# Optimization experiments

Hardware: AMD Instinct MI355X
Metric: run time of the kernel (lower is better)

Reference implementation:

```python
import jax, jax.numpy as jnp
import numpy as np

D_MODEL = 1024
N_EXPERTS = 8
CAPACITY = 2048


def setup_inputs() -> dict:
    key = jax.random.key(0)
    ks = jax.random.split(key, 8)
    D, E, H = D_MODEL, N_EXPERTS, 4 * D_MODEL
    s = lambda fan_in: 1.0 / np.sqrt(fan_in)
    return {
        "x": jax.random.normal(ks[0], (4, 2048, D), dtype=jnp.float32),
        "Wg": jax.random.uniform(ks[1], (D, E), minval=-s(D), maxval=s(D)),
        "bg": jax.random.uniform(ks[2], (E,), minval=-s(D), maxval=s(D)),
        "W1": jax.random.uniform(ks[3], (E, D, H), minval=-s(D), maxval=s(D)),
        "b1": jax.random.uniform(ks[4], (E, H), minval=-s(D), maxval=s(D)),
        "W2": jax.random.uniform(ks[5], (E, H, D), minval=-s(H), maxval=s(H)),
        "b2": jax.random.uniform(ks[6], (E, D), minval=-s(H), maxval=s(H)),
        "top_k": 1,
    }


def reference(x, Wg, bg, W1, b1, W2, b2, top_k):
    B, S, D = x.shape
    E, C = N_EXPERTS, CAPACITY
    x_flat = x.reshape(-1, D)                      # [N, D]
    N = x_flat.shape[0]

    # Router: top-k expert indices per token
    logits = x_flat @ Wg + bg                      # [N, E]
    _, routes = jax.lax.top_k(logits, top_k)       # [N, k]
    r = routes.reshape(-1)                         # [N*k] row-major, matches torch flatten order
    tok = jnp.repeat(jnp.arange(N), top_k)         # token id per routing slot

    # Position of each routed token within its expert's queue (arrival order)
    oh = (r[:, None] == jnp.arange(E)[None, :]).astype(jnp.int32)  # [N*k, E]
    pos = jnp.cumsum(oh, axis=0)[jnp.arange(r.shape[0]), r] - 1    # [N*k]
    kept = pos < C
    slot = jnp.where(kept, pos, C)                 # dropped tokens -> overflow slot C

    # Dispatch: gather tokens into per-expert padded buffers [E, C, D]
    disp = jnp.zeros((E, C + 1, D), dtype=x.dtype).at[r, slot].set(x_flat[tok])
    disp = disp[:, :C]

    # Per-expert MLP (grouped GEMMs)
    h = jax.nn.relu(jnp.einsum('ecd,edh->ech', disp, W1) + b1[:, None, :])
    y = jnp.einsum('ech,ehd->ecd', h, W2) + b2[:, None, :]  # [E, C, D]

    # Combine: scatter expert outputs back; dropped tokens stay zero
    gathered = y[r, jnp.minimum(pos, C - 1)]       # [N*k, D]
    out_flat = jnp.zeros((N, D), dtype=x.dtype).at[tok].set(
        jnp.where(kept[:, None], gathered, 0.0))
    return out_flat.reshape(B, S, D)
```

## Files before the change

kernel.cpp:

```cpp
#include <hip/hip_runtime.h>


#define N_TOK   8192
#define DMODEL  1024
#define HDIM    4096
#define NEXP    8
#define CAP     2048
#define MAXROWS 9216

typedef float  f32x4  __attribute__((ext_vector_type(4)));
typedef __bf16 bf16x8 __attribute__((ext_vector_type(8)));

typedef void __attribute__((address_space(1))) as1_void;
typedef void __attribute__((address_space(3))) as3_void;

__device__ __forceinline__ void async_copy16(void* lds, const void* g) {
    __builtin_amdgcn_global_load_lds((as1_void*)g, (as3_void*)lds, 16, 0, 0);
}

__device__ __forceinline__ unsigned short f2bf(float f) {
    unsigned u = __float_as_uint(f);
    unsigned r = (u + 0x7fffu + ((u >> 16) & 1u)) >> 16;
    return (unsigned short)r;
}

__global__ __launch_bounds__(256) void gate_kernel(
    const float* __restrict__ x, const float* __restrict__ Wg,
    const float* __restrict__ bg, int* __restrict__ route)
{
    const int wave = threadIdx.x >> 6, lane = threadIdx.x & 63;
    const int tok = blockIdx.x * 4 + wave;
    const float* xr = x + (size_t)tok * DMODEL;
    double acc[8];
#pragma unroll
    for (int e = 0; e < 8; ++e) acc[e] = 0.0;
    for (int i = 0; i < DMODEL / 64; ++i) {
        const int d = i * 64 + lane;
        const double xv = (double)xr[d];
        const float* wr = Wg + (size_t)d * 8;
#pragma unroll
        for (int e = 0; e < 8; ++e) acc[e] += xv * (double)wr[e];
    }
#pragma unroll
    for (int e = 0; e < 8; ++e) {
        double v = acc[e];
#pragma unroll
        for (int off = 32; off > 0; off >>= 1) v += __shfl_down(v, off, 64);
        acc[e] = v;
    }
    if (lane == 0) {
        double bv = acc[0] + (double)bg[0];
        int bi = 0;
#pragma unroll
        for (int e = 1; e < 8; ++e) {
            double v = acc[e] + (double)bg[e];
            if (v > bv) { bv = v; bi = e; }
        }
        route[tok] = bi;
    }
}

__global__ __launch_bounds__(256) void scan_kernel(
    const int* __restrict__ route, int* __restrict__ tokrow,
    int* __restrict__ meta)
{
    __shared__ int hist[256][8];
    __shared__ int cntS[8];
    __shared__ int rowbaseS[8];
    const int tid = threadIdx.x;
    for (int i = tid; i < MAXROWS; i += 256) tokrow[i] = -1;
    const int t0 = tid * 32;
    int r[32];
#pragma unroll
    for (int i = 0; i < 32; ++i) r[i] = route[t0 + i];
    int loc[8];
#pragma unroll
    for (int e = 0; e < 8; ++e) loc[e] = 0;
#pragma unroll
    for (int i = 0; i < 32; ++i) {
#pragma unroll
        for (int e = 0; e < 8; ++e) loc[e] += (r[i] == e) ? 1 : 0;
    }
#pragma unroll
    for (int e = 0; e < 8; ++e) hist[tid][e] = loc[e];
    __syncthreads();
    if (tid < 8) {
        int run = 0;
        for (int t = 0; t < 256; ++t) { int v = hist[t][tid]; hist[t][tid] = run; run += v; }
        meta[tid] = run;
        cntS[tid] = run;
    }
    __syncthreads();
    if (tid == 0) {
        int rb = 0;
#pragma unroll
        for (int e = 0; e < 8; ++e) {
            int c = cntS[e]; if (c > CAP) c = CAP;
            int p = (c + 127) & ~127;
            meta[8 + e] = p;
            meta[16 + e] = rb;
            rowbaseS[e] = rb;
            rb += p;
        }
        meta[24] = rb;
    }
    __syncthreads();
    int base[8];
#pragma unroll
    for (int e = 0; e < 8; ++e) base[e] = hist[tid][e];
#pragma unroll
    for (int i = 0; i < 32; ++i) {
        const int e = r[i];
        const int p = base[e]++;
        if (p < CAP) tokrow[rowbaseS[e] + p] = t0 + i;
    }
}

__global__ __launch_bounds__(256) void dispatch_kernel(
    const float* __restrict__ x, const int* __restrict__ tokrow,
    unsigned short* __restrict__ xg)
{
    const int row = blockIdx.x;
    const int tok = tokrow[row];
    const int d = threadIdx.x * 4;
    float4 v = make_float4(0.f, 0.f, 0.f, 0.f);
    if (tok >= 0) v = *(const float4*)(x + (size_t)tok * DMODEL + d);
    ushort4 o;
    o.x = f2bf(v.x); o.y = f2bf(v.y); o.z = f2bf(v.z); o.w = f2bf(v.w);
    *(ushort4*)(xg + (size_t)row * DMODEL + d) = o;
}

__global__ __launch_bounds__(256) void transpose_cast_kernel(
    const float* __restrict__ in, unsigned short* __restrict__ out,
    int R, int C)
{
    __shared__ float t[128][33];
    const size_t base = (size_t)blockIdx.z * R * C;
    const int c0 = blockIdx.x * 32, r0 = blockIdx.y * 128;
    const int x = threadIdx.x, y0 = threadIdx.y;
#pragma unroll
    for (int i = 0; i < 16; ++i) {
        const int r = y0 + i * 8;
        t[r][x] = in[base + (size_t)(r0 + r) * C + c0 + x];
    }
    __syncthreads();
#pragma unroll
    for (int j = 0; j < 4; ++j) {
        const int c = y0 + j * 8;
        ushort4 o;
        o.x = f2bf(t[4 * x + 0][c]);
        o.y = f2bf(t[4 * x + 1][c]);
        o.z = f2bf(t[4 * x + 2][c]);
        o.w = f2bf(t[4 * x + 3][c]);
        *(ushort4*)(&out[base + (size_t)(c0 + c) * R + r0 + 4 * x]) = o;
    }
}

__device__ __forceinline__ void mfma_mainloop(
    const unsigned short* __restrict__ A,
    const unsigned short* __restrict__ B,
    int K, int tid, char* smem, f32x4 acc[4][4])
{
    const int wave = tid >> 6, lane = tid & 63;
    const int mrow = lane >> 2;
    const int kofs = (lane & 3) * 8;
    const int quad = lane >> 4, l16 = lane & 15;
    const int wm = (wave & 1) * 64, wn = (wave >> 1) * 64;

    for (int k0 = 0; k0 < K; k0 += 32) {
        __syncthreads();
#pragma unroll
        for (int i = 0; i < 2; ++i) {
            const int m = wave * 32 + i * 16 + mrow;
            async_copy16(smem + wave * 2048 + i * 1024 + lane * 16,
                         A + (size_t)m * K + k0 + kofs);
        }
#pragma unroll
        for (int i = 0; i < 2; ++i) {
            const int n = wave * 32 + i * 16 + mrow;
            async_copy16(smem + 8192 + wave * 2048 + i * 1024 + lane * 16,
                         B + (size_t)n * K + k0 + kofs);
        }
        __syncthreads();
        bf16x8 a[4], b[4];
#pragma unroll
        for (int mi = 0; mi < 4; ++mi)
            a[mi] = *(const bf16x8*)(smem + ((wm + mi * 16 + l16) * 32 + quad * 8) * 2);
#pragma unroll
        for (int ni = 0; ni < 4; ++ni)
            b[ni] = *(const bf16x8*)(smem + 8192 + ((wn + ni * 16 + l16) * 32 + quad * 8) * 2);
#pragma unroll
        for (int mi = 0; mi < 4; ++mi)
#pragma unroll
            for (int ni = 0; ni < 4; ++ni)
                acc[mi][ni] = __builtin_amdgcn_mfma_f32_16x16x32_bf16(
                    a[mi], b[ni], acc[mi][ni], 0, 0, 0);
    }
}

__global__ __launch_bounds__(256) void gemm1_kernel(
    const unsigned short* __restrict__ xg,
    const unsigned short* __restrict__ wb,
    const float* __restrict__ b1,
    unsigned short* __restrict__ hbuf,
    const int* __restrict__ meta)
{
    const int lin = blockIdx.x + 32 * (blockIdx.y + 16 * blockIdx.z);
    const int work = (lin & 7) * 512 + (lin >> 3);
    const int e = work >> 9;
    const int rem = work & 511;
    const int mtile = rem & 15, ntile = rem >> 4;
    if (mtile * 128 >= meta[8 + e]) return;
    const int row0 = meta[16 + e] + mtile * 128;
    const int tid = threadIdx.x;

    __shared__ __align__(16) char lds[32768];

    f32x4 acc[4][4];
#pragma unroll
    for (int mi = 0; mi < 4; ++mi)
#pragma unroll
        for (int ni = 0; ni < 4; ++ni)
#pragma unroll
            for (int r = 0; r < 4; ++r) acc[mi][ni][r] = 0.0f;

    mfma_mainloop(xg + (size_t)row0 * DMODEL,
                  wb + ((size_t)e * HDIM + (size_t)ntile * 128) * DMODEL,
                  DMODEL, tid, lds, acc);

    __syncthreads();
    unsigned short* hl = (unsigned short*)lds;
    const int wave = tid >> 6, lane = tid & 63;
    const int quad = lane >> 4, l16 = lane & 15;
    const int wm = (wave & 1) * 64, wn = (wave >> 1) * 64;
    const float* bias = b1 + (size_t)e * HDIM + (size_t)ntile * 128;
#pragma unroll
    for (int mi = 0; mi < 4; ++mi)
#pragma unroll
        for (int ni = 0; ni < 4; ++ni) {
            const int cc = wn + ni * 16 + l16;
            const float bv = bias[cc];
#pragma unroll
            for (int r = 0; r < 4; ++r) {
                const int rr = wm + mi * 16 + quad * 4 + r;
                hl[rr * 128 + cc] = f2bf(fmaxf(acc[mi][ni][r] + bv, 0.0f));
            }
        }
    __syncthreads();
#pragma unroll
    for (int i = 0; i < 8; ++i) {
        const int c = tid + i * 256;
        const int m = c >> 4;
        const int nb = (c & 15) * 8;
        *(int4*)(hbuf + (size_t)(row0 + m) * HDIM + (size_t)ntile * 128 + nb) =
            *(const int4*)(hl + m * 128 + nb);
    }
}

__global__ __launch_bounds__(256) void gemm2_kernel(
    const unsigned short* __restrict__ hbuf,
    const unsigned short* __restrict__ wb,
    const float* __restrict__ b2,
    const int* __restrict__ tokrow,
    float* __restrict__ out,
    const int* __restrict__ meta)
{
    const int lin = blockIdx.x + 8 * (blockIdx.y + 16 * blockIdx.z);
    const int work = (lin & 7) * 128 + (lin >> 3);
    const int e = work >> 7;
    const int rem = work & 127;
    const int mtile = rem & 15, ntile = rem >> 4;
    if (mtile * 128 >= meta[8 + e]) return;
    const int row0 = meta[16 + e] + mtile * 128;
    const int tid = threadIdx.x;

    __shared__ __align__(16) char lds[16384];

    f32x4 acc[4][4];
#pragma unroll
    for (int mi = 0; mi < 4; ++mi)
#pragma unroll
        for (int ni = 0; ni < 4; ++ni)
#pragma unroll
            for (int r = 0; r < 4; ++r) acc[mi][ni][r] = 0.0f;

    mfma_mainloop(hbuf + (size_t)row0 * HDIM,
                  wb + ((size_t)e * DMODEL + (size_t)ntile * 128) * HDIM,
                  HDIM, tid, lds, acc);

    const int wave = tid >> 6, lane = tid & 63;
    const int quad = lane >> 4, l16 = lane & 15;
    const int wm = (wave & 1) * 64, wn = (wave >> 1) * 64;
#pragma unroll
    for (int mi = 0; mi < 4; ++mi) {
#pragma unroll
        for (int r = 0; r < 4; ++r) {
            const int rowl = wm + mi * 16 + quad * 4 + r;
            const int tok = tokrow[row0 + rowl];
            if (tok >= 0) {
#pragma unroll
                for (int ni = 0; ni < 4; ++ni) {
                    const int col = ntile * 128 + wn + ni * 16 + l16;
                    out[(size_t)tok * DMODEL + col] =
                        acc[mi][ni][r] + b2[(size_t)e * DMODEL + col];
                }
            }
        }
    }
}

extern "C" void kernel_launch(void* const* d_in, const int* in_sizes, int n_in,
                              void* d_out, int out_size, void* d_ws, size_t ws_size,
                              hipStream_t stream) {
    (void)in_sizes; (void)n_in; (void)out_size; (void)ws_size;
    const float* x  = (const float*)d_in[0];
    const float* Wg = (const float*)d_in[1];
    const float* bg = (const float*)d_in[2];
    const float* W1 = (const float*)d_in[3];
    const float* b1 = (const float*)d_in[4];
    const float* W2 = (const float*)d_in[5];
    const float* b2 = (const float*)d_in[6];
    float* out = (float*)d_out;
    char* ws = (char*)d_ws;

    int* route  = (int*)ws;
    int* tokrow = (int*)(ws + 32768);
    int* meta   = (int*)(ws + 69632);
    unsigned short* xg   = (unsigned short*)(ws + (size_t)131072);
    unsigned short* hbuf = (unsigned short*)(ws + (size_t)20 * 1024 * 1024);
    unsigned short* wb   = (unsigned short*)(ws + (size_t)96 * 1024 * 1024);

    hipMemsetAsync(d_out, 0, (size_t)N_TOK * DMODEL * sizeof(float), stream);

    gate_kernel<<<N_TOK / 4, 256, 0, stream>>>(x, Wg, bg, route);
    scan_kernel<<<1, 256, 0, stream>>>(route, tokrow, meta);
    dispatch_kernel<<<MAXROWS, 256, 0, stream>>>(x, tokrow, xg);

    transpose_cast_kernel<<<dim3(HDIM / 32, DMODEL / 128, NEXP), dim3(32, 8), 0, stream>>>(
        W1, wb, DMODEL, HDIM);
    gemm1_kernel<<<dim3(HDIM / 128, 16, NEXP), 256, 0, stream>>>(
        xg, wb, b1, hbuf, meta);

    transpose_cast_kernel<<<dim3(DMODEL / 32, HDIM / 128, NEXP), dim3(32, 8), 0, stream>>>(
        W2, wb, HDIM, DMODEL);
    gemm2_kernel<<<dim3(DMODEL / 128, 16, NEXP), 256, 0, stream>>>(
        hbuf, wb, b2, tokrow, out, meta);
}
```

Before: 581.1 us.

## Double-buffer GEMM K-loop with BK=64, XOR-swizzled LDS, and vectorized transpose

The shared GEMM mainloop moves from a single 32-wide K tile with two barriers per step to a double-buffered 64-wide K tile. The next tile is loaded asynchronously while the current one is computed, and the LDS layout uses an XOR swizzle to avoid bank conflicts. The weight transpose-cast kernel now uses 64x64 tiles with float4 global loads. LDS per block grows to 64KB, which may reduce occupancy.

Result: slower. 605.1 us (+4.1%).

```diff
diff --git a/kernel.cpp b/kernel.cpp
--- a/kernel.cpp
+++ b/kernel.cpp
@@ -134,25 +134,72 @@
     const float* __restrict__ in, unsigned short* __restrict__ out,
     int R, int C)
 {
-    __shared__ float t[128][33];
+    __shared__ float t[64][65];
     const size_t base = (size_t)blockIdx.z * R * C;
-    const int c0 = blockIdx.x * 32, r0 = blockIdx.y * 128;
-    const int x = threadIdx.x, y0 = threadIdx.y;
-#pragma unroll
-    for (int i = 0; i < 16; ++i) {
-        const int r = y0 + i * 8;
-        t[r][x] = in[base + (size_t)(r0 + r) * C + c0 + x];
-    }
-    __syncthreads();
-#pragma unroll
-    for (int j = 0; j < 4; ++j) {
-        const int c = y0 + j * 8;
+    const int c0 = blockIdx.x * 64, r0 = blockIdx.y * 64;
+    const int tid = threadIdx.x;
+    const int rl = tid >> 4;
+    const int cl = (tid & 15) * 4;
+#pragma unroll
+    for (int i = 0; i < 4; ++i) {
+        const int r = rl + i * 16;
+        const float4 v = *(const float4*)(in + base + (size_t)(r0 + r) * C + c0 + cl);
+        t[r][cl] = v.x; t[r][cl + 1] = v.y; t[r][cl + 2] = v.z; t[r][cl + 3] = v.w;
+    }
+    __syncthreads();
+#pragma unroll
+    for (int i = 0; i < 4; ++i) {
+        const int c = rl + i * 16;
         ushort4 o;
-        o.x = f2bf(t[4 * x + 0][c]);
-        o.y = f2bf(t[4 * x + 1][c]);
-        o.z = f2bf(t[4 * x + 2][c]);
-        o.w = f2bf(t[4 * x + 3][c]);
-        *(ushort4*)(&out[base + (size_t)(c0 + c) * R + r0 + 4 * x]) = o;
+        o.x = f2bf(t[cl + 0][c]);
+        o.y = f2bf(t[cl + 1][c]);
+        o.z = f2bf(t[cl + 2][c]);
+        o.w = f2bf(t[cl + 3][c]);
+        *(ushort4*)(out + base + (size_t)(c0 + c) * R + r0 + cl) = o;
+    }
+}
+
+__device__ __forceinline__ void stage_tile(
+    const unsigned short* __restrict__ A,
+    const unsigned short* __restrict__ B,
+    int K, int tid, char* bufA, char* bufB, int k0)
+{
+#pragma unroll
+    for (int i = 0; i < 4; ++i) {
+        const int c = tid + i * 256;
+        const int row = c >> 3;
+        const int g8 = ((c & 7) ^ (row & 7)) * 8;
+        async_copy16(bufA + (size_t)c * 16, A + (size_t)row * K + k0 + g8);
+    }
+#pragma unroll
+    for (int i = 0; i < 4; ++i) {
+        const int c = tid + i * 256;
+        const int row = c >> 3;
+        const int g8 = ((c & 7) ^ (row & 7)) * 8;
+        async_copy16(bufB + (size_t)c * 16, B + (size_t)row * K + k0 + g8);
+    }
+}
+
+__device__ __forceinline__ void compute_tile(
+    const char* bufA, const char* bufB,
+    int wm, int wn, int l16, int quad, f32x4 acc[4][4])
+{
+#pragma unroll
+    for (int ks = 0; ks < 2; ++ks) {
+        const int sc = ((ks * 4 + quad) ^ (l16 & 7)) * 16;
+        bf16x8 a[4], b[4];
+#pragma unroll
+        for (int mi = 0; mi < 4; ++mi)
+            a[mi] = *(const bf16x8*)(bufA + (wm + mi * 16 + l16) * 128 + sc);
+#pragma unroll
+        for (int ni = 0; ni < 4; ++ni)
+            b[ni] = *(const bf16x8*)(bufB + (wn + ni * 16 + l16) * 128 + sc);
+#pragma unroll
+        for (int mi = 0; mi < 4; ++mi)
+#pragma unroll
+            for (int ni = 0; ni < 4; ++ni)
+                acc[mi][ni] = __builtin_amdgcn_mfma_f32_16x16x32_bf16(
+                    a[mi], b[ni], acc[mi][ni], 0, 0, 0);
     }
 }
 
@@ -162,39 +209,23 @@
     int K, int tid, char* smem, f32x4 acc[4][4])
 {
     const int wave = tid >> 6, lane = tid & 63;
-    const int mrow = lane >> 2;
-    const int kofs = (lane & 3) * 8;
     const int quad = lane >> 4, l16 = lane & 15;
     const int wm = (wave & 1) * 64, wn = (wave >> 1) * 64;
-
-    for (int k0 = 0; k0 < K; k0 += 32) {
+    char* A0 = smem;
+    char* B0 = smem + 16384;
+    char* A1 = smem + 32768;
+    char* B1 = smem + 49152;
+
+    stage_tile(A, B, K, tid, A0, B0, 0);
+    __syncthreads();
+    const int nIter = K >> 6;
+    for (int it = 0; it < nIter; ++it) {
+        const bool odd = (it & 1) != 0;
+        if (it + 1 < nIter)
+            stage_tile(A, B, K, tid, odd ? A0 : A1, odd ? B0 : B1,
+                       (it + 1) << 6);
+        compute_tile(odd ? A1 : A0, odd ? B1 : B0, wm, wn, l16, quad, acc);
         __syncthreads();
-#pragma unroll
-        for (int i = 0; i < 2; ++i) {
-            const int m = wave * 32 + i * 16 + mrow;
-            async_copy16(smem + wave * 2048 + i * 1024 + lane * 16,
-                         A + (size_t)m * K + k0 + kofs);
-        }
-#pragma unroll
-        for (int i = 0; i < 2; ++i) {
-            const int n = wave * 32 + i * 16 + mrow;
-            async_copy16(smem + 8192 + wave * 2048 + i * 1024 + lane * 16,
-                         B + (size_t)n * K + k0 + kofs);
-        }
-        __syncthreads();
-        bf16x8 a[4], b[4];
-#pragma unroll
-        for (int mi = 0; mi < 4; ++mi)
-            a[mi] = *(const bf16x8*)(smem + ((wm + mi * 16 + l16) * 32 + quad * 8) * 2);
-#pragma unroll
-        for (int ni = 0; ni < 4; ++ni)
-            b[ni] = *(const bf16x8*)(smem + 8192 + ((wn + ni * 16 + l16) * 32 + quad * 8) * 2);
-#pragma unroll
-        for (int mi = 0; mi < 4; ++mi)
-#pragma unroll
-            for (int ni = 0; ni < 4; ++ni)
-                acc[mi][ni] = __builtin_amdgcn_mfma_f32_16x16x32_bf16(
-                    a[mi], b[ni], acc[mi][ni], 0, 0, 0);
     }
 }
 
@@ -214,7 +245,7 @@
     const int row0 = meta[16 + e] + mtile * 128;
     const int tid = threadIdx.x;
 
-    __shared__ __align__(16) char lds[32768];
+    __shared__ __align__(16) char lds[65536];
 
     f32x4 acc[4][4];
 #pragma unroll
@@ -228,7 +259,6 @@
                   wb + ((size_t)e * HDIM + (size_t)ntile * 128) * DMODEL,
                   DMODEL, tid, lds, acc);
 
-    __syncthreads();
     unsigned short* hl = (unsigned short*)lds;
     const int wave = tid >> 6, lane = tid & 63;
     const int quad = lane >> 4, l16 = lane & 15;
@@ -274,7 +304,7 @@
     const int row0 = meta[16 + e] + mtile * 128;
     const int tid = threadIdx.x;
 
-    __shared__ __align__(16) char lds[16384];
+    __shared__ __align__(16) char lds[65536];
 
     f32x4 acc[4][4];
 #pragma unroll
@@ -336,12 +366,12 @@
     scan_kernel<<<1, 256, 0, stream>>>(route, tokrow, meta);
     dispatch_kernel<<<MAXROWS, 256, 0, stream>>>(x, tokrow, xg);
 
-    transpose_cast_kernel<<<dim3(HDIM / 32, DMODEL / 128, NEXP), dim3(32, 8), 0, stream>>>(
+    transpose_cast_kernel<<<dim3(HDIM / 64, DMODEL / 64, NEXP), 256, 0, stream>>>(
         W1, wb, DMODEL, HDIM);
     gemm1_kernel<<<dim3(HDIM / 128, 16, NEXP), 256, 0, stream>>>(
         xg, wb, b1, hbuf, meta);
 
-    transpose_cast_kernel<<<dim3(DMODEL / 32, HDIM / 128, NEXP), dim3(32, 8), 0, stream>>>(
+    transpose_cast_kernel<<<dim3(DMODEL / 64, HDIM / 64, NEXP), 256, 0, stream>>>(
         W2, wb, HDIM, DMODEL);
     gemm2_kernel<<<dim3(DMODEL / 128, 16, NEXP), 256, 0, stream>>>(
         hbuf, wb, b2, tokrow, out, meta);
```
